# Kernel tuning notes

Hardware: AMD Instinct MI355X
Metric: run time of the kernel (lower is better)

Reference implementation:

```python
import jax, jax.numpy as jnp
import numpy as np
import itertools

EPSILON = 1e-7
SIGMA_BOOST = 2.0
IN_NUM = 50000
OUT_NUM = 50000
K = 131072
ADDITIONAL = 12
SIGMA_SCALE = 0.2
FEAT = 128
RANK = 2

# floor mask: itertools.product([True, False], repeat=2) -> (4, 2)
FLOOR_MASK = jnp.asarray(
    [[bool(b) for b in bools] for bools in itertools.product([True, False], repeat=RANK)]
)


def setup_inputs() -> dict:
    key = jax.random.key(0)
    k1, k2, k3a, k3b = jax.random.split(key, 4)
    params = jax.random.normal(k1, (K, 4), dtype=jnp.float32)
    x = jax.random.normal(k2, (IN_NUM, FEAT), dtype=jnp.float32)
    # sampled ints: floor(uniform * (1-eps) * rng_dim), per dim
    s0 = jax.random.randint(k3a, (K, ADDITIONAL, 1), 0, OUT_NUM)
    s1 = jax.random.randint(k3b, (K, ADDITIONAL, 1), 0, IN_NUM)
    sampled_ints = jnp.concatenate([s0, s1], axis=-1).astype(jnp.int32)
    return {"params": params, "x": x, "sampled_ints": sampled_ints}


def _hyper(params):
    size = jnp.asarray([OUT_NUM, IN_NUM], dtype=params.dtype)  # (2,)
    means = jax.nn.sigmoid(params[:, 0:RANK]) * (size - 1.0)   # (K, 2)
    sigmas = (jax.nn.softplus(params[:, RANK:RANK + 1] + SIGMA_BOOST) + EPSILON)  # (K, 1)
    sigmas = sigmas * size * SIGMA_SCALE                        # (K, 2)
    values = jax.nn.sigmoid(params[:, RANK + 1])                # (K,)
    return means, sigmas, values


def reference(params, x, sampled_ints):
    means, sigmas, values = _hyper(params)

    # neighbor integer index tuples: floor/ceil combinations -> (K, 4, 2)
    m = means[:, None, :]  # (K, 1, 2)
    neighbor_ints = jnp.where(FLOOR_MASK[None], jnp.floor(m), jnp.ceil(m)).astype(jnp.int32)
    ints = jnp.concatenate([neighbor_ints, sampled_ints], axis=1)  # (K, D, 2)
    ints_fl = ints.astype(means.dtype)

    # unnormalized Gaussian densities of each int tuple under its MVN
    inv_std = jnp.sqrt(1.0 / (EPSILON + sigmas))[:, None, :]      # (K, 1, 2)
    diff = (ints_fl - means[:, None, :]) * inv_std                # (K, D, 2)
    props = jnp.exp(-0.5 * jnp.sum(diff * diff, axis=-1))         # (K, D)
    props = props / jnp.sum(props + EPSILON, axis=1, keepdims=True)

    vals = (values[:, None] * props).reshape(-1)                  # (K*D,)
    i_ixs = ints[:, :, 0].reshape(-1)                             # row indices
    j_ixs = ints[:, :, 1].reshape(-1)                             # col indices

    # sparse (OUT_NUM, IN_NUM) @ x  ->  (OUT_NUM, FEAT)
    gathered = x[j_ixs] * vals[:, None]                           # (nnz, FEAT)
    out = jax.ops.segment_sum(gathered, i_ixs, num_segments=OUT_NUM)
    return out
```

## Files before the change

kernel.cpp:

```cpp
#include <hip/hip_runtime.h>
#include <math.h>

constexpr int KT       = 131072;
constexpr int IN_NUM_C = 50000;
constexpr int OUT_NUM_C= 50000;
constexpr int FEAT_C   = 128;
constexpr int ADD_C    = 12;
constexpr int NP       = 16;
constexpr float EPS    = 1e-7f;
constexpr int CAP      = 128;

__device__ __forceinline__ float xla_expf(float x) {
    const float LOG2EF = 1.44269504088896341f;
    const float C1 =  0.693359375f;
    const float C2 = -2.12194440e-4f;
    const float P0 = 1.9875691500e-4f;
    const float P1 = 1.3981999507e-3f;
    const float P2 = 8.3334519073e-3f;
    const float P3 = 4.1665795894e-2f;
    const float P4 = 1.6666665459e-1f;
    const float P5 = 5.0000001201e-1f;

    const float fx = floorf(__fadd_rn(__fmul_rn(x, LOG2EF), 0.5f));
    const float tmp = __fmul_rn(C1, fx);
    const float z2  = __fmul_rn(C2, fx);
    float r = __fsub_rn(x, tmp);
    r       = __fsub_rn(r, z2);
    const float r2 = __fmul_rn(r, r);

    float y = __fadd_rn(__fmul_rn(r, P0), P1);
    y = __fadd_rn(__fmul_rn(y, r), P2);
    y = __fadd_rn(__fmul_rn(y, r), P3);
    y = __fadd_rn(__fmul_rn(y, r), P4);
    y = __fadd_rn(__fmul_rn(y, r), P5);
    y = __fadd_rn(__fmul_rn(y, r2), r);
    y = __fadd_rn(1.0f, y);

    const int e = (int)fx;
    const float s = __int_as_float((e + 127) << 23);
    const float res = __fmul_rn(y, s);
    return fmaxf(res, x);
}

__device__ __forceinline__ float sigmoid_xla_f32(float p) {
    const float t = xla_expf(-p);
    const float d = __fadd_rn(1.0f, t);
    return __fdiv_rn(1.0f, d);
}


__global__ __launch_bounds__(256) void append_kernel(
    const float* __restrict__ params,
    const int*   __restrict__ samp,
    int*         __restrict__ counts,
    uint2*       __restrict__ sorted)
{
    const int k = blockIdx.x * 16 + (threadIdx.x >> 4);
    const int s = threadIdx.x & 15;

    const float4 p = ((const float4*)params)[k];

    const float m0 = __fmul_rn(sigmoid_xla_f32(p.x), (float)(OUT_NUM_C - 1));
    const float m1 = __fmul_rn(sigmoid_xla_f32(p.y), (float)(IN_NUM_C  - 1));
    const int fl0 = (int)floorf(m0), ce0 = (int)ceilf(m0);
    const int fl1 = (int)floorf(m1), ce1 = (int)ceilf(m1);

    const float z  = p.z + 2.0f;
    const float sp = fmaxf(z, 0.0f) + log1pf(expf(-fabsf(z))) + 1e-7f;
    const float is0 = rsqrtf(1e-7f + sp * (OUT_NUM_C * 0.2f));
    const float is1 = rsqrtf(1e-7f + sp * (IN_NUM_C  * 0.2f));
    const float value = 1.0f / (1.0f + expf(-p.w));

    int iv, jv;
    if (s < 4) {
        iv = (s < 2)        ? fl0 : ce0;
        jv = ((s & 1) == 0) ? fl1 : ce1;
    } else {
        const int base = (k * ADD_C + (s - 4)) * 2;
        iv = samp[base + 0];
        jv = samp[base + 1];
    }
    const float d0 = ((float)iv - m0) * is0;
    const float d1 = ((float)jv - m1) * is1;
    const float prop = expf(-0.5f * (d0 * d0 + d1 * d1));

    float ssum = prop;
    #pragma unroll
    for (int off = 1; off < 16; off <<= 1)
        ssum += __shfl_xor(ssum, off, 64);
    const float denom = ssum + (float)NP * EPS;
    const float w = value * prop / denom;

    if (w != 0.0f) {
        const int pos = atomicAdd(&counts[iv], 1);
        if (pos < CAP)
            sorted[(size_t)iv * CAP + pos] = make_uint2((unsigned)jv, __float_as_uint(w));
    }
}

__global__ __launch_bounds__(256) void gather_cap_kernel(
    const uint2* __restrict__ sorted,
    const int*   __restrict__ counts,
    const float* __restrict__ x,
    float*       __restrict__ out)
{
    const int wv   = threadIdx.x >> 6;
    const int lane = threadIdx.x & 63;
    const int row  = blockIdx.x * 4 + wv;
    const int quad = lane >> 4;
    const int fi   = (lane & 15) << 3;
    const int n    = counts[row];
    const uint2* rowp = sorted + (size_t)row * CAP;

    float4 a0 = make_float4(0.f, 0.f, 0.f, 0.f);
    float4 a1 = make_float4(0.f, 0.f, 0.f, 0.f);

    for (int base = 0; base < n; base += 64) {
        uint2 ent = make_uint2(0u, 0u);
        if (base + lane < n) ent = rowp[base + lane];
        const int m  = min(64, n - base);
        const int mq = (m + 3) >> 2;
        int t = quad;
        #pragma unroll 2
        for (int it = 0; it < mq; ++it, t += 4) {
            const int   j = __shfl((int)ent.x, t, 64);
            const float w = __uint_as_float(__shfl((int)ent.y, t, 64));
            const float* xp = x + (size_t)j * FEAT_C + fi;
            const float4 v0 = *(const float4*)(xp);
            const float4 v1 = *(const float4*)(xp + 4);
            a0.x = fmaf(w, v0.x, a0.x);  a0.y = fmaf(w, v0.y, a0.y);
            a0.z = fmaf(w, v0.z, a0.z);  a0.w = fmaf(w, v0.w, a0.w);
            a1.x = fmaf(w, v1.x, a1.x);  a1.y = fmaf(w, v1.y, a1.y);
            a1.z = fmaf(w, v1.z, a1.z);  a1.w = fmaf(w, v1.w, a1.w);
        }
    }
    #pragma unroll
    for (int off = 16; off < 64; off <<= 1) {
        a0.x += __shfl_xor(a0.x, off, 64);  a0.y += __shfl_xor(a0.y, off, 64);
        a0.z += __shfl_xor(a0.z, off, 64);  a0.w += __shfl_xor(a0.w, off, 64);
        a1.x += __shfl_xor(a1.x, off, 64);  a1.y += __shfl_xor(a1.y, off, 64);
        a1.z += __shfl_xor(a1.z, off, 64);  a1.w += __shfl_xor(a1.w, off, 64);
    }
    if (quad == 0) {
        float* op = out + (size_t)row * FEAT_C + fi;
        *(float4*)(op)     = a0;
        *(float4*)(op + 4) = a1;
    }
}

__global__ __launch_bounds__(256) void hist_kernel(
    const float* __restrict__ params,
    const int*   __restrict__ samp,
    int*         __restrict__ hist)
{
    const int e = blockIdx.x * 256 + threadIdx.x;
    const int k = e >> 4, s = e & 15;
    int iv;
    if (s < 4) {
        const float m0 = __fmul_rn(sigmoid_xla_f32(params[k * 4 + 0]),
                                   (float)(OUT_NUM_C - 1));
        iv = (s < 2) ? (int)floorf(m0) : (int)ceilf(m0);
    } else {
        iv = samp[(k * ADD_C + (s - 4)) * 2];
    }
    atomicAdd(&hist[iv], 1);
}

__global__ __launch_bounds__(1024) void scan_kernel(
    const int* __restrict__ hist,
    int*       __restrict__ offs,
    int*       __restrict__ cursor)
{
    __shared__ int lsum[1024];
    const int t = threadIdx.x;
    const int CH = 49;
    const int lo = t * CH;
    const int hi = min(lo + CH, OUT_NUM_C);
    int s = 0;
    for (int i = lo; i < hi; ++i) s += hist[i];
    lsum[t] = s;
    __syncthreads();
    for (int off = 1; off < 1024; off <<= 1) {
        const int v = (t >= off) ? lsum[t - off] : 0;
        __syncthreads();
        lsum[t] += v;
        __syncthreads();
    }
    int run = (t > 0) ? lsum[t - 1] : 0;
    for (int i = lo; i < hi; ++i) {
        offs[i] = run; cursor[i] = run;
        run += hist[i];
    }
    if (t == 1023) offs[OUT_NUM_C] = lsum[1023];
}

__global__ __launch_bounds__(256) void scatter_kernel(
    const float* __restrict__ params,
    const int*   __restrict__ samp,
    int*         __restrict__ cursor,
    uint2*       __restrict__ sorted)
{
    const int wave = threadIdx.x >> 6;
    const int lane = threadIdx.x & 63;
    const int k    = blockIdx.x * 4 + wave;

    const float p0 = params[k * 4 + 0];
    const float p1 = params[k * 4 + 1];
    const float p2 = params[k * 4 + 2];
    const float p3 = params[k * 4 + 3];

    const float m0 = __fmul_rn(sigmoid_xla_f32(p0), (float)(OUT_NUM_C - 1));
    const float m1 = __fmul_rn(sigmoid_xla_f32(p1), (float)(IN_NUM_C  - 1));
    const int fl0 = (int)floorf(m0), ce0 = (int)ceilf(m0);
    const int fl1 = (int)floorf(m1), ce1 = (int)ceilf(m1);

    const double z  = (double)p2 + 2.0;
    const double sp = fmax(z, 0.0) + log1p(exp(-fabs(z))) + 1e-7;
    const float is0 = (float)sqrt(1.0 / (1e-7 + sp * (OUT_NUM_C * 0.2)));
    const float is1 = (float)sqrt(1.0 / (1e-7 + sp * (IN_NUM_C  * 0.2)));
    const float value = (float)(1.0 / (1.0 + exp(-(double)p3)));

    const int s = lane & 15;
    int iv, jv;
    if (s < 4) {
        iv = (s < 2)        ? fl0 : ce0;
        jv = ((s & 1) == 0) ? fl1 : ce1;
    } else {
        const int base = (k * ADD_C + (s - 4)) * 2;
        iv = samp[base + 0];
        jv = samp[base + 1];
    }
    const float d0 = ((float)iv - m0) * is0;
    const float d1 = ((float)jv - m1) * is1;
    const float prop = expf(-0.5f * (d0 * d0 + d1 * d1));

    float ssum = prop;
    #pragma unroll
    for (int off = 1; off < 64; off <<= 1)
        ssum += __shfl_xor(ssum, off, 64);
    const float denom = ssum * 0.25f + (float)NP * EPS;
    const float w = value * prop / denom;

    if (lane < 16) {
        const int pos = atomicAdd(&cursor[iv], 1);
        sorted[pos] = make_uint2((unsigned)jv, __float_as_uint(w));
    }
}

__global__ __launch_bounds__(64) void gather_kernel(
    const uint2* __restrict__ sorted,
    const int*   __restrict__ offs,
    const float* __restrict__ x,
    float*       __restrict__ out)
{
    const int row  = blockIdx.x;
    const int lane = threadIdx.x;
    const int half = lane >> 5;
    const int fl   = (lane & 31) << 2;
    const int beg = offs[row], end = offs[row + 1];
    float4 acc = make_float4(0.f, 0.f, 0.f, 0.f);
    for (int base = beg; base < end; base += 64) {
        uint2 ent = make_uint2(0u, 0u);
        if (base + lane < end) ent = sorted[base + lane];
        const int n  = min(64, end - base);
        const int nh = (n + 1) >> 1;
        int t = half;
        #pragma unroll 2
        for (int it = 0; it < nh; ++it, t += 2) {
            const int   j = __shfl((int)ent.x, t, 64);
            const float w = __uint_as_float(__shfl((int)ent.y, t, 64));
            const float4 xv = *(const float4*)(x + (size_t)j * FEAT_C + fl);
            acc.x = fmaf(w, xv.x, acc.x);
            acc.y = fmaf(w, xv.y, acc.y);
            acc.z = fmaf(w, xv.z, acc.z);
            acc.w = fmaf(w, xv.w, acc.w);
        }
    }
    acc.x += __shfl_xor(acc.x, 32, 64);
    acc.y += __shfl_xor(acc.y, 32, 64);
    acc.z += __shfl_xor(acc.z, 32, 64);
    acc.w += __shfl_xor(acc.w, 32, 64);
    if (half == 0)
        *(float4*)(out + (size_t)row * FEAT_C + fl) = acc;
}

__global__ __launch_bounds__(256) void mh_scatter_kernel(
    const float* __restrict__ params,
    const float* __restrict__ x,
    const int*   __restrict__ samp,
    float*       __restrict__ out)
{
    const int wave = threadIdx.x >> 6;
    const int lane = threadIdx.x & 63;
    const int k    = blockIdx.x * 4 + wave;

    const float p0 = params[k * 4 + 0];
    const float p1 = params[k * 4 + 1];
    const float p2 = params[k * 4 + 2];
    const float p3 = params[k * 4 + 3];

    const float m0 = __fmul_rn(sigmoid_xla_f32(p0), (float)(OUT_NUM_C - 1));
    const float m1 = __fmul_rn(sigmoid_xla_f32(p1), (float)(IN_NUM_C  - 1));
    const int fl0 = (int)floorf(m0), ce0 = (int)ceilf(m0);
    const int fl1 = (int)floorf(m1), ce1 = (int)ceilf(m1);

    const double z  = (double)p2 + 2.0;
    const double sp = fmax(z, 0.0) + log1p(exp(-fabs(z))) + 1e-7;
    const float is0 = (float)sqrt(1.0 / (1e-7 + sp * (OUT_NUM_C * 0.2)));
    const float is1 = (float)sqrt(1.0 / (1e-7 + sp * (IN_NUM_C  * 0.2)));
    const float value = (float)(1.0 / (1.0 + exp(-(double)p3)));

    const int s = lane & 15;
    int iv, jv;
    if (s < 4) {
        iv = (s < 2)        ? fl0 : ce0;
        jv = ((s & 1) == 0) ? fl1 : ce1;
    } else {
        const int base = (k * ADD_C + (s - 4)) * 2;
        iv = samp[base + 0];
        jv = samp[base + 1];
    }
    const float d0 = ((float)iv - m0) * is0;
    const float d1 = ((float)jv - m1) * is1;
    const float prop = expf(-0.5f * (d0 * d0 + d1 * d1));

    float ssum = prop;
    #pragma unroll
    for (int off = 1; off < 64; off <<= 1)
        ssum += __shfl_xor(ssum, off, 64);
    const float denom = ssum * 0.25f + (float)NP * EPS;
    const float w = value * prop / denom;

    const int f = lane * 2;
    #pragma unroll 1
    for (int t = 0; t < NP; ++t) {
        const float wt = __shfl(w,  t, 64);
        const int   it = __shfl(iv, t, 64);
        const int   jt = __shfl(jv, t, 64);
        const float2 xv = *(const float2*)(x + (size_t)jt * FEAT_C + f);
        float* op = out + (size_t)it * FEAT_C + f;
        atomicAdd(op + 0, xv.x * wt);
        atomicAdd(op + 1, xv.y * wt);
    }
}

extern "C" void kernel_launch(void* const* d_in, const int* in_sizes, int n_in,
                              void* d_out, int out_size, void* d_ws, size_t ws_size,
                              hipStream_t stream)
{
    const float* params = (const float*)d_in[0];
    const float* x      = (const float*)d_in[1];
    const int*   samp   = (const int*)  d_in[2];
    float*       out    = (float*)d_out;

    const size_t CNT_OFF  = 0;
    const size_t BKT_OFF  = 256 * 1024;
    const size_t NEED_CAP = BKT_OFF + (size_t)OUT_NUM_C * CAP * sizeof(uint2);

    const size_t HIST_OFF = 0;
    const size_t OFFS_OFF = 256 * 1024;
    const size_t CURS_OFF = 512 * 1024;
    const size_t SORT_OFF = 768 * 1024;
    const size_t NEED_CS  = SORT_OFF + (size_t)KT * NP * sizeof(uint2);

    if (ws_size >= NEED_CAP) {
        int*   counts = (int*)  ((char*)d_ws + CNT_OFF);
        uint2* sorted = (uint2*)((char*)d_ws + BKT_OFF);
        hipMemsetAsync(counts, 0, OUT_NUM_C * sizeof(int), stream);
        append_kernel    <<<KT / 16,       256, 0, stream>>>(params, samp, counts, sorted);
        gather_cap_kernel<<<OUT_NUM_C / 4, 256, 0, stream>>>(sorted, counts, x, out);
    } else if (ws_size >= NEED_CS) {
        int*   hist   = (int*)  ((char*)d_ws + HIST_OFF);
        int*   offs   = (int*)  ((char*)d_ws + OFFS_OFF);
        int*   cursor = (int*)  ((char*)d_ws + CURS_OFF);
        uint2* sorted = (uint2*)((char*)d_ws + SORT_OFF);
        hipMemsetAsync(hist, 0, (OUT_NUM_C + 1) * sizeof(int), stream);
        hist_kernel   <<<KT * NP / 256, 256,  0, stream>>>(params, samp, hist);
        scan_kernel   <<<1,             1024, 0, stream>>>(hist, offs, cursor);
        scatter_kernel<<<KT / 4,        256,  0, stream>>>(params, samp, cursor, sorted);
        gather_kernel <<<OUT_NUM_C,     64,   0, stream>>>(sorted, offs, x, out);
    } else {
        hipMemsetAsync(out, 0, (size_t)out_size * sizeof(float), stream);
        mh_scatter_kernel<<<KT / 4, 256, 0, stream>>>(params, x, samp, out);
    }
}
```

Before: 128.9 us.

## Compute all 16 entries per thread in append; XCD-aware row remap in gather

The append kernel now gives each parameter row to a single thread instead of a 16-lane group. That thread loads the sampled indices with vector int4 loads, computes all 16 densities, and sums them in registers instead of a shuffle reduction. This cuts the redundant hyperparameter math done by 16 lanes per row, but leaves only 512 blocks with serial atomic appends per thread. The gather kernel remaps block indices so consecutive rows land on the same XCD, improving L2 locality, and it now clamps counts to CAP.

After: 145.4 us. 12.8% more time.

```diff
diff --git a/kernel.cpp b/kernel.cpp
--- a/kernel.cpp
+++ b/kernel.cpp
@@ -55,8 +55,7 @@
     int*         __restrict__ counts,
     uint2*       __restrict__ sorted)
 {
-    const int k = blockIdx.x * 16 + (threadIdx.x >> 4);
-    const int s = threadIdx.x & 15;
+    const int k = blockIdx.x * 256 + threadIdx.x;
 
     const float4 p = ((const float4*)params)[k];
 
@@ -71,30 +70,50 @@
     const float is1 = rsqrtf(1e-7f + sp * (IN_NUM_C  * 0.2f));
     const float value = 1.0f / (1.0f + expf(-p.w));
 
-    int iv, jv;
-    if (s < 4) {
-        iv = (s < 2)        ? fl0 : ce0;
-        jv = ((s & 1) == 0) ? fl1 : ce1;
-    } else {
-        const int base = (k * ADD_C + (s - 4)) * 2;
-        iv = samp[base + 0];
-        jv = samp[base + 1];
-    }
-    const float d0 = ((float)iv - m0) * is0;
-    const float d1 = ((float)jv - m1) * is1;
-    const float prop = expf(-0.5f * (d0 * d0 + d1 * d1));
-
-    float ssum = prop;
-    #pragma unroll
-    for (int off = 1; off < 16; off <<= 1)
-        ssum += __shfl_xor(ssum, off, 64);
-    const float denom = ssum + (float)NP * EPS;
-    const float w = value * prop / denom;
-
-    if (w != 0.0f) {
-        const int pos = atomicAdd(&counts[iv], 1);
-        if (pos < CAP)
-            sorted[(size_t)iv * CAP + pos] = make_uint2((unsigned)jv, __float_as_uint(w));
+    int4 sv[6];
+    const int4* sp4 = (const int4*)(samp + (size_t)k * (2 * ADD_C));
+    #pragma unroll
+    for (int t = 0; t < 6; ++t) sv[t] = sp4[t];
+
+    int ivs[NP], jvs[NP];
+    ivs[0] = fl0; jvs[0] = fl1;
+    ivs[1] = fl0; jvs[1] = ce1;
+    ivs[2] = ce0; jvs[2] = fl1;
+    ivs[3] = ce0; jvs[3] = ce1;
+    #pragma unroll
+    for (int t = 0; t < 6; ++t) {
+        ivs[4 + 2*t]     = sv[t].x;  jvs[4 + 2*t]     = sv[t].y;
+        ivs[4 + 2*t + 1] = sv[t].z;  jvs[4 + 2*t + 1] = sv[t].w;
+    }
+
+    float props[NP];
+    #pragma unroll
+    for (int e = 0; e < NP; ++e) {
+        const float d0 = ((float)ivs[e] - m0) * is0;
+        const float d1 = ((float)jvs[e] - m1) * is1;
+        props[e] = expf(-0.5f * (d0 * d0 + d1 * d1));
+    }
+
+    float s1[8], s2[4], s3[2];
+    #pragma unroll
+    for (int i = 0; i < 8; ++i) s1[i] = props[2*i] + props[2*i + 1];
+    #pragma unroll
+    for (int i = 0; i < 4; ++i) s2[i] = s1[2*i] + s1[2*i + 1];
+    s3[0] = s2[0] + s2[1];
+    s3[1] = s2[2] + s2[3];
+    const float denom = (s3[0] + s3[1]) + (float)NP * EPS;
+    const float vd = value / denom;
+
+    #pragma unroll
+    for (int e = 0; e < NP; ++e) {
+        const float w = vd * props[e];
+        if (w != 0.0f) {
+            const int iv = ivs[e];
+            const int pos = atomicAdd(&counts[iv], 1);
+            if (pos < CAP)
+                sorted[(size_t)iv * CAP + pos] =
+                    make_uint2((unsigned)jvs[e], __float_as_uint(w));
+        }
     }
 }
 
@@ -104,12 +123,19 @@
     const float* __restrict__ x,
     float*       __restrict__ out)
 {
+    const int nwg = gridDim.x;
+    const int q   = nwg >> 3, r = nwg & 7;
+    const int xcd = blockIdx.x & 7, lin = blockIdx.x >> 3;
+    const int b   = (xcd < r ? xcd * (q + 1)
+                             : r * (q + 1) + (xcd - r) * q) + lin;
+
     const int wv   = threadIdx.x >> 6;
     const int lane = threadIdx.x & 63;
-    const int row  = blockIdx.x * 4 + wv;
+    const int row  = b * 4 + wv;
     const int quad = lane >> 4;
     const int fi   = (lane & 15) << 3;
-    const int n    = counts[row];
+    int n = counts[row];
+    if (n > CAP) n = CAP;
     const uint2* rowp = sorted + (size_t)row * CAP;
 
     float4 a0 = make_float4(0.f, 0.f, 0.f, 0.f);
@@ -367,7 +393,7 @@
         int*   counts = (int*)  ((char*)d_ws + CNT_OFF);
         uint2* sorted = (uint2*)((char*)d_ws + BKT_OFF);
         hipMemsetAsync(counts, 0, OUT_NUM_C * sizeof(int), stream);
-        append_kernel    <<<KT / 16,       256, 0, stream>>>(params, samp, counts, sorted);
+        append_kernel    <<<KT / 256,      256, 0, stream>>>(params, samp, counts, sorted);
         gather_cap_kernel<<<OUT_NUM_C / 4, 256, 0, stream>>>(sorted, counts, x, out);
     } else if (ws_size >= NEED_CS) {
         int*   hist   = (int*)  ((char*)d_ws + HIST_OFF);
```
